# Optimization experiments

Hardware: AMD Instinct MI355X
Metric: run time of the kernel (lower is better)

The kernel has to match this reference:

```python
import jax, jax.numpy as jnp
import numpy as np

NUM_GROUPS = 32
NUM_HEADS = 8
EPS = 1e-5


def group_norm(x, gamma, beta):
    B, C, H, W = x.shape
    g = NUM_GROUPS
    xg = x.reshape(B, g, C // g, H, W)
    mean = xg.mean(axis=(2, 3, 4), keepdims=True)
    var = xg.var(axis=(2, 3, 4), keepdims=True)
    xn = ((xg - mean) * jax.lax.rsqrt(var + EPS)).reshape(B, C, H, W)
    return xn * gamma[None, :, None, None] + beta[None, :, None, None]


def setup_inputs() -> dict:
    key = jax.random.key(0)
    ks = jax.random.split(key, 7)
    B, C, H, W = 16, 512, 32, 32
    x = jax.random.normal(ks[0], (B, C, H, W), dtype=jnp.float32)
    norm_w = jnp.ones((C,), jnp.float32)
    norm_b = jnp.zeros((C,), jnp.float32)
    s1 = 1.0 / np.sqrt(C)
    qkv_w = jax.random.uniform(ks[1], (3 * C, C), jnp.float32, -s1, s1)
    qkv_b = jax.random.uniform(ks[2], (3 * C,), jnp.float32, -s1, s1)
    proj_w = jax.random.uniform(ks[3], (C, C), jnp.float32, -s1, s1)
    proj_b = jax.random.uniform(ks[4], (C,), jnp.float32, -s1, s1)
    return {"x": x, "norm_w": norm_w, "norm_b": norm_b,
            "qkv_w": qkv_w, "qkv_b": qkv_b,
            "proj_w": proj_w, "proj_b": proj_b}


def reference(x, norm_w, norm_b, qkv_w, qkv_b, proj_w, proj_b):
    B, C, H, W = x.shape
    nh = NUM_HEADS
    hd = C // nh
    S = H * W
    h = group_norm(x, norm_w, norm_b)
    # 1x1 conv == channel matmul: [B,3C,H,W]
    qkv = jnp.einsum('oc,bchw->bohw', qkv_w, h) + qkv_b[None, :, None, None]
    q, k, v = jnp.split(qkv, 3, axis=1)
    # q,v -> [B, nh, S, hd]; k -> [B, nh, hd, S]
    q = q.reshape(B, nh, hd, S).transpose(0, 1, 3, 2)
    k = k.reshape(B, nh, hd, S)
    v = v.reshape(B, nh, hd, S).transpose(0, 1, 3, 2)
    scale = 1.0 / np.sqrt(hd)
    attn = jnp.einsum('bhsd,bhdt->bhst', q, k) * scale
    attn = jax.nn.softmax(attn, axis=-1)
    out = jnp.einsum('bhst,bhtd->bhsd', attn, v)  # [B,nh,S,hd]
    out = out.transpose(0, 1, 3, 2).reshape(B, C, H, W)
    out = jnp.einsum('oc,bchw->bohw', proj_w, out) + proj_b[None, :, None, None]
    return out + x
```

## Files before the change

### kernel.cpp

```cpp
#include <hip/hip_runtime.h>
#include <hip/hip_bf16.h>
#include <stdint.h>

#define B_N 16
#define C_N 512
#define S_N 1024
#define G_N 32
#define NH  8
#define HD  64

typedef __attribute__((ext_vector_type(8))) short bf16x8;
typedef __attribute__((ext_vector_type(4))) float f32x4;
typedef __attribute__((ext_vector_type(16))) float f32x16;
typedef unsigned short u16;
typedef unsigned int   u32;
typedef __attribute__((ext_vector_type(4))) u16 u16x4;
typedef __attribute__((ext_vector_type(4))) u32 u32x4;

#define SC2F 0.18033688011112042f

__device__ __forceinline__ u16 f2bf(float f) {
  u32 u = __builtin_bit_cast(u32, f);
  u32 r = (u + 0x7fffu + ((u >> 16) & 1u)) >> 16;
  return (u16)r;
}

__device__ __forceinline__ u32 pk2(float a, float b) {
  __hip_bfloat162 h = __float22bfloat162_rn(make_float2(a, b));
  u32 r; __builtin_memcpy(&r, &h, 4);
  return r;
}

__device__ __forceinline__ void gll16(const void* g, void* l) {
  __builtin_amdgcn_global_load_lds((const __attribute__((address_space(1))) u32*)g,
                                   (__attribute__((address_space(3))) u32*)l, 16, 0, 0);
}

__global__ __launch_bounds__(256) void gn_stats(const float* __restrict__ x,
                                                float* __restrict__ stats) {
  const int bg = blockIdx.x;
  const float4* xv = (const float4*)(x + (size_t)bg * (16 * S_N));
  float s = 0.f, ss = 0.f;
  for (int i = threadIdx.x; i < 4096; i += 256) {
    float4 v = xv[i];
    s  += v.x + v.y + v.z + v.w;
    ss += v.x*v.x + v.y*v.y + v.z*v.z + v.w*v.w;
  }
  #pragma unroll
  for (int m = 1; m < 64; m <<= 1) { s += __shfl_xor(s, m); ss += __shfl_xor(ss, m); }
  __shared__ float red[2][4];
  const int wid = threadIdx.x >> 6;
  if ((threadIdx.x & 63) == 0) { red[0][wid] = s; red[1][wid] = ss; }
  __syncthreads();
  if (threadIdx.x == 0) {
    float S1 = red[0][0]+red[0][1]+red[0][2]+red[0][3];
    float S2 = red[1][0]+red[1][1]+red[1][2]+red[1][3];
    float mean = S1 * (1.f/16384.f);
    float var  = S2 * (1.f/16384.f) - mean*mean;
    stats[bg*2]   = mean;
    stats[bg*2+1] = rsqrtf(var + 1e-5f);
  }
}

__global__ __launch_bounds__(256) void gn_apply_t(const float* __restrict__ x,
                                                  const float* __restrict__ stats,
                                                  const float* __restrict__ nw,
                                                  const float* __restrict__ nb,
                                                  u16* __restrict__ h_t) {
  const int c0 = blockIdx.x * 32, s0 = blockIdx.y * 64, b = blockIdx.z;
  __shared__ u16 tile[32][68];
  const int t = threadIdx.x;
  #pragma unroll
  for (int i = 0; i < 2; i++) {
    int idx4 = (i*256 + t) * 4;
    int cr = idx4 >> 6, sr = idx4 & 63;
    int c = c0 + cr;
    float4 v = *(const float4*)&x[((size_t)b*C_N + c)*S_N + s0 + sr];
    int bg = b*G_N + (c >> 4);
    float mean = stats[bg*2], rstd = stats[bg*2+1];
    float w = nw[c]*rstd;
    float bb = nb[c] - mean*w;
    tile[cr][sr]   = f2bf(v.x*w + bb);
    tile[cr][sr+1] = f2bf(v.y*w + bb);
    tile[cr][sr+2] = f2bf(v.z*w + bb);
    tile[cr][sr+3] = f2bf(v.w*w + bb);
  }
  __syncthreads();
  #pragma unroll
  for (int i = 0; i < 2; i++) {
    int idx = i*256 + t;
    int sr = idx >> 3;
    int cr4 = (idx & 7) * 4;
    u16x4 v = { tile[cr4][sr], tile[cr4+1][sr], tile[cr4+2][sr], tile[cr4+3][sr] };
    *(u16x4*)&h_t[((size_t)b*S_N + s0 + sr)*C_N + c0 + cr4] = v;
  }
}

__global__ __launch_bounds__(256) void cvt_bf16_k(const float* __restrict__ src,
                                                  u16* __restrict__ dst, int n4) {
  int i = blockIdx.x*256 + threadIdx.x;
  if (i < n4) {
    float4 v = ((const float4*)src)[i];
    u16x4 r = { f2bf(v.x), f2bf(v.y), f2bf(v.z), f2bf(v.w) };
    ((u16x4*)dst)[i] = r;
  }
}

__global__ __launch_bounds__(256) void gemm_qkv(const u16* __restrict__ h_t,
                                                const u16* __restrict__ wq,
                                                const float* __restrict__ bq,
                                                u16* __restrict__ Qp,
                                                u16* __restrict__ Kp,
                                                u16* __restrict__ Vp) {
  __shared__ u16 Ash[128*32];
  __shared__ u16 Bsh[128*32];
  const int n0 = blockIdx.x*128, m0 = blockIdx.y*128, b = blockIdx.z;
  const int tid = threadIdx.x, wid = tid >> 6, lane = tid & 63;
  const int wm = wid >> 1, wn = wid & 1;
  const u16* Ag = h_t + (size_t)b*S_N*C_N;
  const f32x4 vzero = {0.f,0.f,0.f,0.f};
  f32x4 acc[4][4];
  #pragma unroll
  for (int i=0;i<4;i++)
    #pragma unroll
    for (int j=0;j<4;j++) acc[i][j] = vzero;

  const int arow = lane >> 2, aslot = (lane & 3) * 8;
  for (int k0 = 0; k0 < C_N; k0 += 32) {
    __syncthreads();
    #pragma unroll
    for (int i = 0; i < 2; i++) {
      int r = wid*32 + i*16 + arow;
      gll16(Ag + (size_t)(m0+r)*C_N + k0 + aslot, &Ash[(wid*32+i*16)*32]);
      gll16(wq + (size_t)(n0+r)*C_N + k0 + aslot, &Bsh[(wid*32+i*16)*32]);
    }
    __syncthreads();
    bf16x8 aF[4], bF[4];
    #pragma unroll
    for (int mi=0;mi<4;mi++)
      aF[mi] = *(const bf16x8*)&Ash[(wm*64+mi*16+(lane&15))*32 + (lane>>4)*8];
    #pragma unroll
    for (int ni=0;ni<4;ni++)
      bF[ni] = *(const bf16x8*)&Bsh[(wn*64+ni*16+(lane&15))*32 + (lane>>4)*8];
    #pragma unroll
    for (int mi=0;mi<4;mi++)
      #pragma unroll
      for (int ni=0;ni<4;ni++)
        acc[mi][ni] = __builtin_amdgcn_mfma_f32_16x16x32_bf16(aF[mi], bF[ni], acc[mi][ni], 0, 0, 0);
  }

  #pragma unroll
  for (int mi=0;mi<4;mi++) {
    #pragma unroll
    for (int ni=0;ni<4;ni++) {
      int o = n0 + wn*64 + ni*16 + (lane & 15);
      float bias = bq[o];
      int sec = o >> 9;
      int oo  = o & 511;
      int hh  = oo >> 6, d = oo & 63;
      size_t bh = (size_t)(b*NH + hh);
      float qsc = (sec == 0) ? SC2F : 1.0f;
      #pragma unroll
      for (int r=0;r<4;r++) {
        int s = m0 + wm*64 + mi*16 + (lane>>4)*4 + r;
        u16 bv = f2bf((acc[mi][ni][r] + bias) * qsc);
        if (sec == 0)      Qp[(bh*S_N + s)*HD + d] = bv;
        else if (sec == 1) Kp[(bh*S_N + s)*HD + d] = bv;
        else               Vp[(bh*HD + d)*S_N + s] = bv;
      }
    }
  }
}

__global__ __launch_bounds__(256) void attn_fwd(const u16* __restrict__ Qp,
                                                const u16* __restrict__ Kp,
                                                const u16* __restrict__ Vp,
                                                u16* __restrict__ at) {
  __shared__ u16 Kl[2][64*64];
  __shared__ u16 Vl[2][64*64];
  const int hh = blockIdx.x, q0 = blockIdx.y*128, b = blockIdx.z;
  const int tid = threadIdx.x, wid = tid >> 6, lane = tid & 63;
  const int l31 = lane & 31, hi = lane >> 5;
  const size_t bh = (size_t)(b*NH + hh);
  const u16* Qb = Qp + bh*(S_N*HD);
  const u16* Kb = Kp + bh*(S_N*HD);
  const u16* Vb = Vp + bh*(HD*S_N);
  const int s = q0 + wid*32 + l31;

  bf16x8 qf[4];
  #pragma unroll
  for (int kt=0;kt<4;kt++)
    qf[kt] = *(const bf16x8*)&Qb[(size_t)s*HD + kt*16 + hi*8];

  f32x16 oacc[2];
  #pragma unroll
  for (int dt=0;dt<2;dt++)
    #pragma unroll
    for (int i=0;i<16;i++) oacc[dt][i] = 0.f;
  float l_run = 0.f;

  const int ra = wid*16 + (lane >> 3);
  const int rb = ra + 8;
  const int ca = (((lane & 7) ^ (ra & 7)) * 8);
  const int cb = (((lane & 7) ^ (rb & 7)) * 8);

  gll16(Kb + (size_t)ra*HD + ca,  &Kl[0][(wid*16    )*64]);
  gll16(Kb + (size_t)rb*HD + cb,  &Kl[0][(wid*16 + 8)*64]);
  gll16(Vb + (size_t)ra*S_N + ca, &Vl[0][(wid*16    )*64]);
  gll16(Vb + (size_t)rb*S_N + cb, &Vl[0][(wid*16 + 8)*64]);

  int cur = 0;
  #pragma unroll 1
  for (int it = 0; it < 16; ++it) {
    const int t0 = it * 64;
    asm volatile("s_waitcnt vmcnt(0)" ::: "memory");
    __syncthreads();

    if (it < 15) {
      const int tn = t0 + 64;
      gll16(Kb + (size_t)(tn + ra)*HD + ca, &Kl[cur^1][(wid*16    )*64]);
      gll16(Kb + (size_t)(tn + rb)*HD + cb, &Kl[cur^1][(wid*16 + 8)*64]);
      gll16(Vb + (size_t)ra*S_N + tn + ca,  &Vl[cur^1][(wid*16    )*64]);
      gll16(Vb + (size_t)rb*S_N + tn + cb,  &Vl[cur^1][(wid*16 + 8)*64]);
    }

    bf16x8 kF[2][4];
    #pragma unroll
    for (int tt=0;tt<2;tt++)
      #pragma unroll
      for (int kt=0;kt<4;kt++) {
        int row = tt*32 + l31;
        int phys = (kt*2 + hi) ^ (row & 7);
        kF[tt][kt] = *(const bf16x8*)&Kl[cur][row*64 + phys*8];
      }

    f32x16 st[2];
    #pragma unroll
    for (int tt=0;tt<2;tt++)
      #pragma unroll
      for (int i=0;i<16;i++) st[tt][i] = 0.f;
    __builtin_amdgcn_s_setprio(1);
    #pragma unroll
    for (int tt=0;tt<2;tt++)
      #pragma unroll
      for (int kt=0;kt<4;kt++)
        st[tt] = __builtin_amdgcn_mfma_f32_32x32x16_bf16(kF[tt][kt], qf[kt], st[tt], 0, 0, 0);
    __builtin_amdgcn_s_setprio(0);

    #pragma unroll
    for (int tt=0;tt<2;tt++)
      #pragma unroll
      for (int i=0;i<16;i++)
        st[tt][i] = exp2f(st[tt][i]);

    float sm[16];
    #pragma unroll
    for (int i=0;i<16;i++) sm[i] = st[0][i] + st[1][i];
    #pragma unroll
    for (int off=8; off; off>>=1)
      #pragma unroll
      for (int i=0;i<8;i++) if (i < off) sm[i] += sm[i+off];
    l_run += sm[0];

    u32x4 paw[4];
    #pragma unroll
    for (int ks=0;ks<4;ks++) {
      float p0 = st[ks>>1][(ks&1)*8+0], p1 = st[ks>>1][(ks&1)*8+1];
      float p2 = st[ks>>1][(ks&1)*8+2], p3 = st[ks>>1][(ks&1)*8+3];
      float p4 = st[ks>>1][(ks&1)*8+4], p5 = st[ks>>1][(ks&1)*8+5];
      float p6 = st[ks>>1][(ks&1)*8+6], p7 = st[ks>>1][(ks&1)*8+7];
      u32 w0 = pk2(p0, p1);
      u32 w1 = pk2(p2, p3);
      u32 w2 = pk2(p4, p5);
      u32 w3 = pk2(p6, p7);
      u32 s0 = hi ? w0 : w2;
      u32 s1 = hi ? w1 : w3;
      u32 r0 = (u32)__shfl_xor((int)s0, 32);
      u32 r1 = (u32)__shfl_xor((int)s1, 32);
      u32x4 w = { hi ? r0 : w0, hi ? r1 : w1, hi ? w2 : r0, hi ? w3 : r1 };
      paw[ks] = w;
    }

    __builtin_amdgcn_s_setprio(1);
    #pragma unroll
    for (int dt=0;dt<2;dt++)
      #pragma unroll
      for (int ks=0;ks<4;ks++) {
        int row = dt*32 + l31;
        int phys = (ks*2 + hi) ^ (row & 7);
        bf16x8 vF = *(const bf16x8*)&Vl[cur][row*64 + phys*8];
        oacc[dt] = __builtin_amdgcn_mfma_f32_32x32x16_bf16(vF, __builtin_bit_cast(bf16x8, paw[ks]), oacc[dt], 0, 0, 0);
      }
    __builtin_amdgcn_s_setprio(0);

    __syncthreads();
    cur ^= 1;
  }

  l_run += __shfl_xor(l_run, 32);
  float inv = 1.0f / l_run;
  #pragma unroll
  for (int dt=0;dt<2;dt++)
    #pragma unroll
    for (int qd=0;qd<4;qd++) {
      int dbase = 4*hi + 8*qd + 32*dt;
      u16x4 o;
      #pragma unroll
      for (int j=0;j<4;j++) o[j] = f2bf(oacc[dt][qd*4+j] * inv);
      *(u16x4*)&at[((size_t)b*S_N + s)*C_N + hh*HD + dbase] = o;
    }
}

__global__ __launch_bounds__(256) void gemm_proj(const u16* __restrict__ pwb,
                                                 const u16* __restrict__ at,
                                                 const float* __restrict__ bp,
                                                 const float* __restrict__ x,
                                                 float* __restrict__ out) {
  __shared__ u16 Ash[128*32];
  __shared__ u16 Bsh[128*32];
  const int n0 = blockIdx.x*128, m0 = blockIdx.y*128, b = blockIdx.z;
  const int tid = threadIdx.x, wid = tid >> 6, lane = tid & 63;
  const int wm = wid >> 1, wn = wid & 1;
  const u16* Bg = at + (size_t)b*S_N*C_N;
  const f32x4 vzero = {0.f,0.f,0.f,0.f};
  f32x4 acc[4][4];
  #pragma unroll
  for (int i=0;i<4;i++)
    #pragma unroll
    for (int j=0;j<4;j++) acc[i][j] = vzero;

  const int arow = lane >> 2, aslot = (lane & 3) * 8;
  for (int k0 = 0; k0 < C_N; k0 += 32) {
    __syncthreads();
    #pragma unroll
    for (int i = 0; i < 2; i++) {
      int r = wid*32 + i*16 + arow;
      gll16(pwb + (size_t)(m0+r)*C_N + k0 + aslot, &Ash[(wid*32+i*16)*32]);
      gll16(Bg  + (size_t)(n0+r)*C_N + k0 + aslot, &Bsh[(wid*32+i*16)*32]);
    }
    __syncthreads();
    bf16x8 aF[4], bF[4];
    #pragma unroll
    for (int mi=0;mi<4;mi++)
      aF[mi] = *(const bf16x8*)&Ash[(wm*64+mi*16+(lane&15))*32 + (lane>>4)*8];
    #pragma unroll
    for (int ni=0;ni<4;ni++)
      bF[ni] = *(const bf16x8*)&Bsh[(wn*64+ni*16+(lane&15))*32 + (lane>>4)*8];
    #pragma unroll
    for (int mi=0;mi<4;mi++)
      #pragma unroll
      for (int ni=0;ni<4;ni++)
        acc[mi][ni] = __builtin_amdgcn_mfma_f32_16x16x32_bf16(aF[mi], bF[ni], acc[mi][ni], 0, 0, 0);
  }

  #pragma unroll
  for (int mi=0;mi<4;mi++) {
    #pragma unroll
    for (int ni=0;ni<4;ni++) {
      int ss = n0 + wn*64 + ni*16 + (lane & 15);
      #pragma unroll
      for (int r=0;r<4;r++) {
        int o = m0 + wm*64 + mi*16 + (lane>>4)*4 + r;
        size_t idx = ((size_t)b*C_N + o)*S_N + ss;
        out[idx] = acc[mi][ni][r] + bp[o] + x[idx];
      }
    }
  }
}

extern "C" void kernel_launch(void* const* d_in, const int* in_sizes, int n_in,
                              void* d_out, int out_size, void* d_ws, size_t ws_size,
                              hipStream_t stream) {
  const float* x     = (const float*)d_in[0];
  const float* nw    = (const float*)d_in[1];
  const float* nb    = (const float*)d_in[2];
  const float* qkvw  = (const float*)d_in[3];
  const float* qkvb  = (const float*)d_in[4];
  const float* projw = (const float*)d_in[5];
  const float* projb = (const float*)d_in[6];
  float* out = (float*)d_out;

  char* ws = (char*)d_ws;
  float* stats = (float*)ws;
  u16* h_t = (u16*)(ws + 4096);
  u16* qw  = (u16*)(ws + 4096 + 16777216);
  u16* pw  = (u16*)((char*)qw + 1572864);
  u16* Qp  = (u16*)((char*)pw + 524288);
  u16* Kp  = (u16*)((char*)Qp + 16777216);
  u16* Vp  = (u16*)((char*)Kp + 16777216);
  u16* at  = (u16*)((char*)Vp + 16777216);

  gn_stats  <<<512, 256, 0, stream>>>(x, stats);
  gn_apply_t<<<dim3(16,16,16), 256, 0, stream>>>(x, stats, nw, nb, h_t);
  cvt_bf16_k<<<768, 256, 0, stream>>>(qkvw, qw, 196608);
  cvt_bf16_k<<<256, 256, 0, stream>>>(projw, pw, 65536);
  gemm_qkv  <<<dim3(12,8,16), 256, 0, stream>>>(h_t, qw, qkvb, Qp, Kp, Vp);
  attn_fwd  <<<dim3(8,8,16), 256, 0, stream>>>(Qp, Kp, Vp, at);
  gemm_proj <<<dim3(8,4,16), 256, 0, stream>>>(pw, at, projb, x, out);
}
```

Baseline: 266.7 us.

## Compute softmax row sums via ones-MFMA, unroll attention loop, merge weight casts

The attention kernel now builds the softmax denominator with an extra MFMA against a ones vector, replacing the per-lane shuffle-and-add reduction. It also packs P with the v_cvt_pk_bf16_f32 instruction and unrolls the KV loop by two so the double-buffer indices become compile-time constants. The two weight-conversion launches are merged into one kernel. The denominator now sums the bf16-rounded P values rather than fp32 ones, which shifts numerics slightly, and each tile costs four extra MFMAs.

```diff
diff --git a/kernel.cpp b/kernel.cpp
--- a/kernel.cpp
+++ b/kernel.cpp
@@ -25,9 +25,9 @@
   return (u16)r;
 }
 
-__device__ __forceinline__ u32 pk2(float a, float b) {
-  __hip_bfloat162 h = __float22bfloat162_rn(make_float2(a, b));
-  u32 r; __builtin_memcpy(&r, &h, 4);
+__device__ __forceinline__ u32 cvtpk(float a, float b) {
+  u32 r;
+  asm("v_cvt_pk_bf16_f32 %0, %1, %2" : "=v"(r) : "v"(a), "v"(b));
   return r;
 }
 
@@ -96,14 +96,17 @@
   }
 }
 
-__global__ __launch_bounds__(256) void cvt_bf16_k(const float* __restrict__ src,
-                                                  u16* __restrict__ dst, int n4) {
+__global__ __launch_bounds__(256) void cvt_bf16_all(const float* __restrict__ qkvw,
+                                                    const float* __restrict__ projw,
+                                                    u16* __restrict__ qw,
+                                                    u16* __restrict__ pw) {
   int i = blockIdx.x*256 + threadIdx.x;
-  if (i < n4) {
-    float4 v = ((const float4*)src)[i];
-    u16x4 r = { f2bf(v.x), f2bf(v.y), f2bf(v.z), f2bf(v.w) };
-    ((u16x4*)dst)[i] = r;
-  }
+  const float4* src; u16x4* dst; int j;
+  if (i < 196608) { src = (const float4*)qkvw; dst = (u16x4*)qw; j = i; }
+  else            { src = (const float4*)projw; dst = (u16x4*)pw; j = i - 196608; }
+  float4 v = src[j];
+  u16x4 r = { f2bf(v.x), f2bf(v.y), f2bf(v.z), f2bf(v.w) };
+  dst[j] = r;
 }
 
 __global__ __launch_bounds__(256) void gemm_qkv(const u16* __restrict__ h_t,
@@ -172,6 +175,92 @@
   }
 }
 
+__device__ __forceinline__ void attn_tile_body(const u16* __restrict__ Kb,
+                                               const u16* __restrict__ Vb,
+                                               u16* __restrict__ KlC, u16* __restrict__ VlC,
+                                               u16* __restrict__ KlN, u16* __restrict__ VlN,
+                                               const bf16x8 (&qf)[4], const bf16x8 onesf,
+                                               f32x16 (&oacc)[2], f32x16& oacc_l,
+                                               int it, int l31, int hi,
+                                               int ra, int rb, int ca, int cb, int wid) {
+  const int t0 = it * 64;
+  asm volatile("s_waitcnt vmcnt(0)" ::: "memory");
+  __syncthreads();
+
+  if (it < 15) {
+    const int tn = t0 + 64;
+    gll16(Kb + (size_t)(tn + ra)*HD + ca, &KlN[(wid*16    )*64]);
+    gll16(Kb + (size_t)(tn + rb)*HD + cb, &KlN[(wid*16 + 8)*64]);
+    gll16(Vb + (size_t)ra*S_N + tn + ca,  &VlN[(wid*16    )*64]);
+    gll16(Vb + (size_t)rb*S_N + tn + cb,  &VlN[(wid*16 + 8)*64]);
+  }
+
+  bf16x8 kF[2][4];
+  #pragma unroll
+  for (int tt=0;tt<2;tt++)
+    #pragma unroll
+    for (int kt=0;kt<4;kt++) {
+      int row = tt*32 + l31;
+      int phys = (kt*2 + hi) ^ (row & 7);
+      kF[tt][kt] = *(const bf16x8*)&KlC[row*64 + phys*8];
+    }
+
+  f32x16 st[2];
+  #pragma unroll
+  for (int tt=0;tt<2;tt++)
+    #pragma unroll
+    for (int i=0;i<16;i++) st[tt][i] = 0.f;
+  __builtin_amdgcn_s_setprio(1);
+  #pragma unroll
+  for (int tt=0;tt<2;tt++)
+    #pragma unroll
+    for (int kt=0;kt<4;kt++)
+      st[tt] = __builtin_amdgcn_mfma_f32_32x32x16_bf16(kF[tt][kt], qf[kt], st[tt], 0, 0, 0);
+  __builtin_amdgcn_s_setprio(0);
+
+  #pragma unroll
+  for (int tt=0;tt<2;tt++)
+    #pragma unroll
+    for (int i=0;i<16;i++)
+      st[tt][i] = exp2f(st[tt][i]);
+
+  u32x4 paw[4];
+  #pragma unroll
+  for (int ks=0;ks<4;ks++) {
+    float p0 = st[ks>>1][(ks&1)*8+0], p1 = st[ks>>1][(ks&1)*8+1];
+    float p2 = st[ks>>1][(ks&1)*8+2], p3 = st[ks>>1][(ks&1)*8+3];
+    float p4 = st[ks>>1][(ks&1)*8+4], p5 = st[ks>>1][(ks&1)*8+5];
+    float p6 = st[ks>>1][(ks&1)*8+6], p7 = st[ks>>1][(ks&1)*8+7];
+    u32 w0 = cvtpk(p0, p1);
+    u32 w1 = cvtpk(p2, p3);
+    u32 w2 = cvtpk(p4, p5);
+    u32 w3 = cvtpk(p6, p7);
+    u32 s0 = hi ? w0 : w2;
+    u32 s1 = hi ? w1 : w3;
+    u32 r0 = (u32)__shfl_xor((int)s0, 32);
+    u32 r1 = (u32)__shfl_xor((int)s1, 32);
+    u32x4 w = { hi ? r0 : w0, hi ? r1 : w1, hi ? w2 : r0, hi ? w3 : r1 };
+    paw[ks] = w;
+  }
+
+  __builtin_amdgcn_s_setprio(1);
+  #pragma unroll
+  for (int ks=0;ks<4;ks++) {
+    bf16x8 pb = __builtin_bit_cast(bf16x8, paw[ks]);
+    oacc_l = __builtin_amdgcn_mfma_f32_32x32x16_bf16(onesf, pb, oacc_l, 0, 0, 0);
+    #pragma unroll
+    for (int dt=0;dt<2;dt++) {
+      int row = dt*32 + l31;
+      int phys = (ks*2 + hi) ^ (row & 7);
+      bf16x8 vF = *(const bf16x8*)&VlC[row*64 + phys*8];
+      oacc[dt] = __builtin_amdgcn_mfma_f32_32x32x16_bf16(vF, pb, oacc[dt], 0, 0, 0);
+    }
+  }
+  __builtin_amdgcn_s_setprio(0);
+
+  __syncthreads();
+}
+
 __global__ __launch_bounds__(256) void attn_fwd(const u16* __restrict__ Qp,
                                                 const u16* __restrict__ Kp,
                                                 const u16* __restrict__ Vp,
@@ -192,12 +281,16 @@
   for (int kt=0;kt<4;kt++)
     qf[kt] = *(const bf16x8*)&Qb[(size_t)s*HD + kt*16 + hi*8];
 
-  f32x16 oacc[2];
+  const u32x4 onesw = {0x3F803F80u, 0x3F803F80u, 0x3F803F80u, 0x3F803F80u};
+  const bf16x8 onesf = __builtin_bit_cast(bf16x8, onesw);
+
+  f32x16 oacc[2], oacc_l;
   #pragma unroll
   for (int dt=0;dt<2;dt++)
     #pragma unroll
     for (int i=0;i<16;i++) oacc[dt][i] = 0.f;
-  float l_run = 0.f;
+  #pragma unroll
+  for (int i=0;i<16;i++) oacc_l[i] = 0.f;
 
   const int ra = wid*16 + (lane >> 3);
   const int rb = ra + 8;
@@ -209,96 +302,15 @@
   gll16(Vb + (size_t)ra*S_N + ca, &Vl[0][(wid*16    )*64]);
   gll16(Vb + (size_t)rb*S_N + cb, &Vl[0][(wid*16 + 8)*64]);
 
-  int cur = 0;
   #pragma unroll 1
-  for (int it = 0; it < 16; ++it) {
-    const int t0 = it * 64;
-    asm volatile("s_waitcnt vmcnt(0)" ::: "memory");
-    __syncthreads();
-
-    if (it < 15) {
-      const int tn = t0 + 64;
-      gll16(Kb + (size_t)(tn + ra)*HD + ca, &Kl[cur^1][(wid*16    )*64]);
-      gll16(Kb + (size_t)(tn + rb)*HD + cb, &Kl[cur^1][(wid*16 + 8)*64]);
-      gll16(Vb + (size_t)ra*S_N + tn + ca,  &Vl[cur^1][(wid*16    )*64]);
-      gll16(Vb + (size_t)rb*S_N + tn + cb,  &Vl[cur^1][(wid*16 + 8)*64]);
-    }
-
-    bf16x8 kF[2][4];
-    #pragma unroll
-    for (int tt=0;tt<2;tt++)
-      #pragma unroll
-      for (int kt=0;kt<4;kt++) {
-        int row = tt*32 + l31;
-        int phys = (kt*2 + hi) ^ (row & 7);
-        kF[tt][kt] = *(const bf16x8*)&Kl[cur][row*64 + phys*8];
-      }
-
-    f32x16 st[2];
-    #pragma unroll
-    for (int tt=0;tt<2;tt++)
-      #pragma unroll
-      for (int i=0;i<16;i++) st[tt][i] = 0.f;
-    __builtin_amdgcn_s_setprio(1);
-    #pragma unroll
-    for (int tt=0;tt<2;tt++)
-      #pragma unroll
-      for (int kt=0;kt<4;kt++)
-        st[tt] = __builtin_amdgcn_mfma_f32_32x32x16_bf16(kF[tt][kt], qf[kt], st[tt], 0, 0, 0);
-    __builtin_amdgcn_s_setprio(0);
-
-    #pragma unroll
-    for (int tt=0;tt<2;tt++)
-      #pragma unroll
-      for (int i=0;i<16;i++)
-        st[tt][i] = exp2f(st[tt][i]);
-
-    float sm[16];
-    #pragma unroll
-    for (int i=0;i<16;i++) sm[i] = st[0][i] + st[1][i];
-    #pragma unroll
-    for (int off=8; off; off>>=1)
-      #pragma unroll
-      for (int i=0;i<8;i++) if (i < off) sm[i] += sm[i+off];
-    l_run += sm[0];
-
-    u32x4 paw[4];
-    #pragma unroll
-    for (int ks=0;ks<4;ks++) {
-      float p0 = st[ks>>1][(ks&1)*8+0], p1 = st[ks>>1][(ks&1)*8+1];
-      float p2 = st[ks>>1][(ks&1)*8+2], p3 = st[ks>>1][(ks&1)*8+3];
-      float p4 = st[ks>>1][(ks&1)*8+4], p5 = st[ks>>1][(ks&1)*8+5];
-      float p6 = st[ks>>1][(ks&1)*8+6], p7 = st[ks>>1][(ks&1)*8+7];
-      u32 w0 = pk2(p0, p1);
-      u32 w1 = pk2(p2, p3);
-      u32 w2 = pk2(p4, p5);
-      u32 w3 = pk2(p6, p7);
-      u32 s0 = hi ? w0 : w2;
-      u32 s1 = hi ? w1 : w3;
-      u32 r0 = (u32)__shfl_xor((int)s0, 32);
-      u32 r1 = (u32)__shfl_xor((int)s1, 32);
-      u32x4 w = { hi ? r0 : w0, hi ? r1 : w1, hi ? w2 : r0, hi ? w3 : r1 };
-      paw[ks] = w;
-    }
-
-    __builtin_amdgcn_s_setprio(1);
-    #pragma unroll
-    for (int dt=0;dt<2;dt++)
-      #pragma unroll
-      for (int ks=0;ks<4;ks++) {
-        int row = dt*32 + l31;
-        int phys = (ks*2 + hi) ^ (row & 7);
-        bf16x8 vF = *(const bf16x8*)&Vl[cur][row*64 + phys*8];
-        oacc[dt] = __builtin_amdgcn_mfma_f32_32x32x16_bf16(vF, __builtin_bit_cast(bf16x8, paw[ks]), oacc[dt], 0, 0, 0);
-      }
-    __builtin_amdgcn_s_setprio(0);
-
-    __syncthreads();
-    cur ^= 1;
-  }
-
-  l_run += __shfl_xor(l_run, 32);
-  float inv = 1.0f / l_run;
+  for (int it = 0; it < 16; it += 2) {
+    attn_tile_body(Kb, Vb, Kl[0], Vl[0], Kl[1], Vl[1], qf, onesf, oacc, oacc_l,
+                   it,     l31, hi, ra, rb, ca, cb, wid);
+    attn_tile_body(Kb, Vb, Kl[1], Vl[1], Kl[0], Vl[0], qf, onesf, oacc, oacc_l,
+                   it + 1, l31, hi, ra, rb, ca, cb, wid);
+  }
+
+  float inv = 1.0f / oacc_l[0];
   #pragma unroll
   for (int dt=0;dt<2;dt++)
     #pragma unroll
@@ -390,11 +402,10 @@
   u16* Vp  = (u16*)((char*)Kp + 16777216);
   u16* at  = (u16*)((char*)Vp + 16777216);
 
-  gn_stats  <<<512, 256, 0, stream>>>(x, stats);
-  gn_apply_t<<<dim3(16,16,16), 256, 0, stream>>>(x, stats, nw, nb, h_t);
-  cvt_bf16_k<<<768, 256, 0, stream>>>(qkvw, qw, 196608);
-  cvt_bf16_k<<<256, 256, 0, stream>>>(projw, pw, 65536);
-  gemm_qkv  <<<dim3(12,8,16), 256, 0, stream>>>(h_t, qw, qkvb, Qp, Kp, Vp);
-  attn_fwd  <<<dim3(8,8,16), 256, 0, stream>>>(Qp, Kp, Vp, at);
-  gemm_proj <<<dim3(8,4,16), 256, 0, stream>>>(pw, at, projb, x, out);
-}
+  gn_stats    <<<512, 256, 0, stream>>>(x, stats);
+  gn_apply_t  <<<dim3(16,16,16), 256, 0, stream>>>(x, stats, nw, nb, h_t);
+  cvt_bf16_all<<<1024, 256, 0, stream>>>(qkvw, projw, qw, pw);
+  gemm_qkv    <<<dim3(12,8,16), 256, 0, stream>>>(h_t, qw, qkvb, Qp, Kp, Vp);
+  attn_fwd    <<<dim3(8,8,16), 256, 0, stream>>>(Qp, Kp, Vp, at);
+  gemm_proj   <<<dim3(8,4,16), 256, 0, stream>>>(pw, at, projb, x, out);
+}
```

Result: faster. 256.3 us (-3.9%).
